# Performance work log

Hardware: AMD Instinct MI355X
Metric: run time of the kernel (lower is better)

The kernel has to match this reference:

```python
import jax, jax.numpy as jnp
import numpy as np

DIM = 1024
NUM_HEADS = 16
HEAD_DIM = DIM // NUM_HEADS
MLP_DIM = 4 * DIM
EPS = 1e-5


def layer_norm(x, g, b):
    mu = jnp.mean(x, axis=-1, keepdims=True)
    var = jnp.mean(jnp.square(x - mu), axis=-1, keepdims=True)
    return (x - mu) * jax.lax.rsqrt(var + EPS) * g + b


def setup_inputs() -> dict:
    key = jax.random.key(0)
    ks = jax.random.split(key, 12)
    B, L = 2, 2048
    s = lambda n: 1.0 / np.sqrt(n)
    return {
        "x": jax.random.normal(ks[0], (B, L, DIM), jnp.float32),
        "attn_mask": jnp.tril(jnp.ones((L, L), jnp.int32))[None, None],  # [1,1,L,L]
        "w_qkv": jax.random.normal(ks[1], (DIM, 3 * DIM), jnp.float32) * s(DIM),
        "b_qkv": jnp.zeros((3 * DIM,), jnp.float32),
        "w_proj": jax.random.normal(ks[2], (DIM, DIM), jnp.float32) * s(DIM),
        "b_proj": jnp.zeros((DIM,), jnp.float32),
        "w_fc1": jax.random.normal(ks[3], (DIM, MLP_DIM), jnp.float32) * s(DIM),
        "b_fc1": jnp.zeros((MLP_DIM,), jnp.float32),
        "w_fc2": jax.random.normal(ks[4], (MLP_DIM, DIM), jnp.float32) * s(MLP_DIM),
        "b_fc2": jnp.zeros((DIM,), jnp.float32),
        "g1": jnp.ones((DIM,), jnp.float32),
        "beta1": jnp.zeros((DIM,), jnp.float32),
        "g2": jnp.ones((DIM,), jnp.float32),
        "beta2": jnp.zeros((DIM,), jnp.float32),
    }


def reference(x, attn_mask, w_qkv, b_qkv, w_proj, b_proj, w_fc1, b_fc1,
              w_fc2, b_fc2, g1, beta1, g2, beta2):
    B, L, D = x.shape
    scale = HEAD_DIM ** -0.5

    # --- attention branch (pre-norm) ---
    h = layer_norm(x, g1, beta1)
    qkv = h @ w_qkv + b_qkv                                  # [B,L,3D]
    qkv = qkv.reshape(B, L, 3, NUM_HEADS, HEAD_DIM)
    q = qkv[:, :, 0].transpose(0, 2, 1, 3)                   # [B,H,L,hd]
    k = qkv[:, :, 1].transpose(0, 2, 1, 3)
    v = qkv[:, :, 2].transpose(0, 2, 1, 3)
    attn = jnp.einsum('bhqd,bhkd->bhqk', q, k) * scale       # [B,H,L,L]
    attn = jnp.where(attn_mask == 0, -jnp.inf, attn)
    attn = jax.nn.softmax(attn, axis=-1)
    y = jnp.einsum('bhqk,bhkd->bhqd', attn, v)               # [B,H,L,hd]
    y = y.transpose(0, 2, 1, 3).reshape(B, L, D)
    y = y @ w_proj + b_proj
    x = x + y

    # --- MLP branch (pre-norm) ---
    h = layer_norm(x, g2, beta2)
    h = jax.nn.gelu(h @ w_fc1 + b_fc1, approximate=False)
    h = h @ w_fc2 + b_fc2
    return x + h
```

## Files before the change

kernel.cpp:

```cpp
#include <hip/hip_runtime.h>
#include <hip/hip_bf16.h>
#include <stdint.h>

typedef unsigned short u16;
typedef __attribute__((ext_vector_type(8))) short bf16x8;
typedef __attribute__((ext_vector_type(4))) short bf16x4;
typedef __attribute__((ext_vector_type(4))) float f32x4;
typedef __attribute__((ext_vector_type(16))) float f32x16;
typedef __attribute__((ext_vector_type(4))) unsigned short u16x4;

#define DEVI static __device__ __forceinline__

DEVI u16 f2bf(float f) {
    unsigned int u = __builtin_bit_cast(unsigned int, f);
    return (u16)((u + 0x7fffu + ((u >> 16) & 1u)) >> 16);
}

DEVI float gelu_f(float v) {
    const float z = 1.5957691216f * (v + 0.044715f * v * v * v);
    return v / (1.0f + __expf(-z));
}

DEVI void async_copy16(const void* g, void* l) {
    __builtin_amdgcn_global_load_lds((const __attribute__((address_space(1))) void*)g,
                                     (__attribute__((address_space(3))) void*)l,
                                     16, 0, 0);
}

__global__ __launch_bounds__(256) void tcvt_kernel(const float* __restrict__ src,
                                                   u16* __restrict__ dst,
                                                   int K, int N) {
    __shared__ float tile[32][33];
    const int k0 = blockIdx.x * 32, n0 = blockIdx.y * 32;
    const int t = threadIdx.x;
    const int c = t & 31, r0 = t >> 5;
#pragma unroll
    for (int p = 0; p < 4; ++p) {
        const int r = r0 + p * 8;
        tile[r][c] = src[(size_t)(k0 + r) * N + n0 + c];
    }
    __syncthreads();
#pragma unroll
    for (int p = 0; p < 4; ++p) {
        const int r = r0 + p * 8;
        dst[(size_t)(n0 + r) * K + k0 + c] = f2bf(tile[c][r]);
    }
}

__global__ __launch_bounds__(256) void ln_kernel(const float* __restrict__ x,
                                                 const float* __restrict__ gw,
                                                 const float* __restrict__ bw,
                                                 u16* __restrict__ out) {
    const int row = blockIdx.x;
    const int t = threadIdx.x;
    const float4 v = ((const float4*)(x + (size_t)row * 1024))[t];
    float s  = v.x + v.y + v.z + v.w;
    float ss = v.x * v.x + v.y * v.y + v.z * v.z + v.w * v.w;
#pragma unroll
    for (int off = 32; off > 0; off >>= 1) {
        s  += __shfl_down(s, off);
        ss += __shfl_down(ss, off);
    }
    __shared__ float red[8];
    const int wv = t >> 6;
    if ((t & 63) == 0) { red[wv] = s; red[4 + wv] = ss; }
    __syncthreads();
    if (t == 0) {
        red[0] = red[0] + red[1] + red[2] + red[3];
        red[4] = red[4] + red[5] + red[6] + red[7];
    }
    __syncthreads();
    const float mean = red[0] * (1.0f / 1024.0f);
    const float var  = red[4] * (1.0f / 1024.0f) - mean * mean;
    const float rstd = rsqrtf(var + 1e-5f);
    const float4 gv = ((const float4*)gw)[t];
    const float4 bv = ((const float4*)bw)[t];
    u16x4 o;
    o[0] = f2bf((v.x - mean) * rstd * gv.x + bv.x);
    o[1] = f2bf((v.y - mean) * rstd * gv.y + bv.y);
    o[2] = f2bf((v.z - mean) * rstd * gv.z + bv.z);
    o[3] = f2bf((v.w - mean) * rstd * gv.w + bv.w);
    ((u16x4*)out)[(size_t)row * 256 + t] = o;
}

DEVI void stage64(const char* g, size_t ldb, char* lds0, int lane, int wv) {
    const int colsw = ((lane & 3) << 4) ^ (lane & 32);
    const int rl = lane >> 2;
#pragma unroll
    for (int i = 0; i < 4; ++i) {
        const int s = wv * 4 + i;
        const int kh = s >> 3, c = s & 7;
        async_copy16(g + (size_t)(c * 16 + rl) * ldb + kh * 64 + colsw,
                     lds0 + s * 1024);
    }
}

template <int EPI, int SPLITK>
__global__ __launch_bounds__(256, 4) void gemmv6(const u16* __restrict__ A,
                                                 const u16* __restrict__ Bt,
                                                 const float* __restrict__ bias,
                                                 void* __restrict__ out0,
                                                 void* __restrict__ out1,
                                                 void* __restrict__ out2,
                                                 int M, int N, int K) {
    __shared__ __align__(16) char As[16384];
    __shared__ __align__(16) char Bs[16384];
    const int tid = threadIdx.x;
    const int lane = tid & 63, wv = tid >> 6;
    const int wr = wv >> 1, wc = wv & 1;
    const int g = lane >> 4, qq = lane & 15;
    const int rdoff = qq * 64 + ((g * 16) ^ ((qq & 8) << 2));

    const int nwg = gridDim.x;
    int id = blockIdx.x;
    id = (id & 7) * (nwg >> 3) + (id >> 3);
    const int MT = M >> 7, NTn = N >> 7;
    const int slice = id / (MT * NTn);
    const int r2 = id % (MT * NTn);
    const int m0 = (r2 % MT) << 7;
    const int n0 = (r2 / MT) << 7;
    const int Ks = K / SPLITK;
    const int NT = Ks >> 6;
    const size_t ldb = (size_t)K * 2;

    const char* pa = (const char*)A + (size_t)m0 * ldb + (size_t)slice * Ks * 2;
    const char* pb = (const char*)Bt + (size_t)n0 * ldb + (size_t)slice * Ks * 2;

    f32x4 acc[4][4] = {};

    for (int t = 0; t < NT; ++t) {
        stage64(pa + (size_t)t * 128, ldb, As, lane, wv);
        stage64(pb + (size_t)t * 128, ldb, Bs, lane, wv);
        __syncthreads();
#pragma unroll
        for (int kh = 0; kh < 2; ++kh) {
            bf16x8 fa[4], fb[4];
#pragma unroll
            for (int fn = 0; fn < 4; ++fn)
                fb[fn] = *(const bf16x8*)(Bs + (kh * 8 + wc * 4 + fn) * 1024 + rdoff);
#pragma unroll
            for (int fm = 0; fm < 4; ++fm)
                fa[fm] = *(const bf16x8*)(As + (kh * 8 + wr * 4 + fm) * 1024 + rdoff);
#pragma unroll
            for (int fm = 0; fm < 4; ++fm)
#pragma unroll
                for (int fn = 0; fn < 4; ++fn)
                    acc[fm][fn] = __builtin_amdgcn_mfma_f32_16x16x32_bf16(fa[fm], fb[fn],
                                                                          acc[fm][fn], 0, 0, 0);
        }
        __syncthreads();
    }

#pragma unroll
    for (int fm = 0; fm < 4; ++fm) {
#pragma unroll
        for (int fn = 0; fn < 4; ++fn) {
            const int mrow = m0 + wr * 64 + fm * 16 + g * 4;
            const int ncol = n0 + wc * 64 + fn * 16 + qq;
            if constexpr (EPI == 0) {
                const float bs = bias[ncol];
                const int sec = ncol >> 10;
                const int hd_ = ncol & 1023;
                const int hh = hd_ >> 6, dd = hd_ & 63;
                if (sec == 2) {
                    const int b_ = mrow >> 11, l_ = mrow & 2047;
                    u16x4 pk;
#pragma unroll
                    for (int r = 0; r < 4; ++r) pk[r] = f2bf(acc[fm][fn][r] + bs);
                    *(u16x4*)((u16*)out2 + ((size_t)((b_ * 16 + hh) * 64 + dd)) * 2048 + l_) = pk;
                } else {
                    u16* dst = (sec == 0) ? (u16*)out0 : (u16*)out1;
                    const float sc = (sec == 0) ? 0.1803368801f : 1.0f;
#pragma unroll
                    for (int r = 0; r < 4; ++r) {
                        const int mr = mrow + r;
                        const int b_ = mr >> 11, l_ = mr & 2047;
                        dst[((size_t)((b_ * 16 + hh) * 2048 + l_)) * 64 + dd] =
                            f2bf((acc[fm][fn][r] + bs) * sc);
                    }
                }
            } else if constexpr (EPI == 2) {
                const float bs = bias[ncol];
                u16* dst = (u16*)out0;
#pragma unroll
                for (int r = 0; r < 4; ++r)
                    dst[(size_t)(mrow + r) * N + ncol] = f2bf(gelu_f(acc[fm][fn][r] + bs));
            } else {
                float* dst = (float*)out0 + (size_t)slice * M * N;
#pragma unroll
                for (int r = 0; r < 4; ++r)
                    dst[(size_t)(mrow + r) * N + ncol] = acc[fm][fn][r];
            }
        }
    }
}

template <int SPLIT>
__global__ __launch_bounds__(256) void reduceN_kernel(const float* __restrict__ p,
                                                      const float* __restrict__ bias,
                                                      const float* __restrict__ res,
                                                      float* __restrict__ out,
                                                      int MN4, int N4) {
    const int i = blockIdx.x * 256 + threadIdx.x;
    float4 s = ((const float4*)p)[i];
#pragma unroll
    for (int s2 = 1; s2 < SPLIT; ++s2) {
        const float4 q = ((const float4*)p)[(size_t)s2 * MN4 + i];
        s.x += q.x; s.y += q.y; s.z += q.z; s.w += q.w;
    }
    const float4 r = ((const float4*)res)[i];
    const float4 bs = ((const float4*)bias)[i & (N4 - 1)];
    float4 o;
    o.x = s.x + r.x + bs.x;
    o.y = s.y + r.y + bs.y;
    o.z = s.z + r.z + bs.z;
    o.w = s.w + r.w + bs.w;
    ((float4*)out)[i] = o;
}

DEVI void stage_kv(const char* kbase, const char* vbase, int key0,
                   u16* ksm, u16* vsm, int wv, int lane) {
#pragma unroll
    for (int i = 0; i < 2; ++i) {
        const int c = wv + i * 4;
        const int off = c * 1024 + lane * 16;
        const int row = off >> 7;
        const int scol = (off & 127) ^ ((row & 7) << 4);
        async_copy16(kbase + (size_t)key0 * 128 + (size_t)row * 128 + scol,
                     (char*)ksm + c * 1024);
    }
#pragma unroll
    for (int i = 0; i < 2; ++i) {
        const int c = wv + i * 4;
        const int row = c * 8 + (lane >> 3);
        const int scol = ((lane & 7) * 16) ^ ((row & 7) << 4);
        async_copy16(vbase + (size_t)row * 4096 + (size_t)key0 * 2 + scol,
                     (char*)vsm + c * 1024);
    }
}

__global__ __launch_bounds__(256, 4) void attn32_seg(const u16* __restrict__ Q,
                                                     const u16* __restrict__ Kk,
                                                     const u16* __restrict__ Vt,
                                                     float* __restrict__ opart,
                                                     float2* __restrict__ ml) {
    const int bh = blockIdx.z;
    const int seg = blockIdx.y;
    const int qb = gridDim.x - 1 - blockIdx.x;
    const int tid = threadIdx.x;
    const int wv = tid >> 6, lane = tid & 63;
    const int hi = lane >> 5, qc = lane & 31;

    __shared__ __align__(16) u16 Ksm[4096];
    __shared__ __align__(16) u16 Vsm[4096];
    __shared__ __align__(16) u16 Pl[4][32 * 68];

    const char* Kb = (const char*)(Kk + (size_t)bh * 2048 * 64);
    const char* Vb = (const char*)(Vt + (size_t)bh * 64 * 2048);
    u16* Pw = &Pl[wv][0];

    const int q0w = qb * 128 + wv * 32;
    const int qg = q0w + qc;
    const int nt_half = qb + 1;
    const int kt_begin = seg ? nt_half : 0;
    const int kt_end = seg ? (2 * qb + 2) : nt_half;
    const int ntw = min(kt_end, 2 * qb + (wv >> 1) + 1);

    bf16x8 qf[4];
    {
        const u16* Qp = Q + ((size_t)bh * 2048 + qg) * 64;
#pragma unroll
        for (int c = 0; c < 4; ++c)
            qf[c] = *(const bf16x8*)(Qp + c * 16 + hi * 8);
    }

    f32x16 oacc[2];
#pragma unroll
    for (int r = 0; r < 16; ++r) { oacc[0][r] = 0.0f; oacc[1][r] = 0.0f; }
    float m_run = -60000.0f, l_run = 0.0f;

    for (int kt = kt_begin; kt < kt_end; ++kt) {
        const int key0 = kt * 64;
        stage_kv(Kb, Vb, key0, Ksm, Vsm, wv, lane);
        __syncthreads();
        if (kt < ntw) {
            f32x16 sacc[2];
#pragma unroll
            for (int r = 0; r < 16; ++r) { sacc[0][r] = 0.0f; sacc[1][r] = 0.0f; }
#pragma unroll
            for (int c = 0; c < 4; ++c) {
#pragma unroll
                for (int kb = 0; kb < 2; ++kb) {
                    const int kr = kb * 32 + qc;
                    const bf16x8 ak = *(const bf16x8*)((const char*)Ksm + kr * 128 +
                                          ((c * 32 + hi * 16) ^ ((kr & 7) << 4)));
                    sacc[kb] = __builtin_amdgcn_mfma_f32_32x32x16_bf16(ak, qf[c],
                                                                       sacc[kb], 0, 0, 0);
                }
            }
            float pmax = -1e30f;
            if (key0 + 63 > q0w) {
#pragma unroll
                for (int kb = 0; kb < 2; ++kb)
#pragma unroll
                    for (int r = 0; r < 16; ++r) {
                        const int key = key0 + kb * 32 + (r & 3) + 8 * (r >> 2) + 4 * hi;
                        float s = sacc[kb][r];
                        if (key > qg) s = -1e30f;
                        sacc[kb][r] = s;
                        pmax = fmaxf(pmax, s);
                    }
            } else {
#pragma unroll
                for (int kb = 0; kb < 2; ++kb)
#pragma unroll
                    for (int r = 0; r < 16; ++r) pmax = fmaxf(pmax, sacc[kb][r]);
            }
            pmax = fmaxf(pmax, __shfl_xor(pmax, 32));
            if (pmax > m_run + 11.0f) {
                const float alpha = __builtin_amdgcn_exp2f(m_run - pmax);
#pragma unroll
                for (int r = 0; r < 16; ++r) { oacc[0][r] *= alpha; oacc[1][r] *= alpha; }
                l_run *= alpha;
                m_run = pmax;
            }
            float lsum = 0.0f;
#pragma unroll
            for (int kb = 0; kb < 2; ++kb)
#pragma unroll
                for (int j = 0; j < 4; ++j) {
                    u16x4 pk4;
#pragma unroll
                    for (int t = 0; t < 4; ++t) {
                        const float e = __builtin_amdgcn_exp2f(sacc[kb][j * 4 + t] - m_run);
                        lsum += e;
                        pk4[t] = f2bf(e);
                    }
                    *(u16x4*)(Pw + qc * 68 + kb * 32 + j * 8 + 4 * hi) = pk4;
                }
            lsum += __shfl_xor(lsum, 32);
            l_run += lsum;
#pragma unroll
            for (int c = 0; c < 4; ++c) {
                const u16* pp = Pw + qc * 68 + c * 16 + hi * 8;
                union { bf16x8 v; struct { bf16x4 lo; bf16x4 hi2; } s; } u;
                u.s.lo  = *(const bf16x4*)(pp);
                u.s.hi2 = *(const bf16x4*)(pp + 4);
                const bf16x8 pf = u.v;
#pragma unroll
                for (int db = 0; db < 2; ++db) {
                    const int dr = db * 32 + qc;
                    const bf16x8 av = *(const bf16x8*)((const char*)Vsm + dr * 128 +
                                          ((c * 32 + hi * 16) ^ ((dr & 7) << 4)));
                    oacc[db] = __builtin_amdgcn_mfma_f32_32x32x16_bf16(av, pf,
                                                                       oacc[db], 0, 0, 0);
                }
            }
        }
        __syncthreads();
    }

    const size_t row = (size_t)seg * 65536 + (size_t)bh * 2048 + qg;
    float* op = opart + row * 64;
#pragma unroll
    for (int db = 0; db < 2; ++db)
#pragma unroll
        for (int j = 0; j < 4; ++j) {
            float4 v;
            v.x = oacc[db][j * 4 + 0];
            v.y = oacc[db][j * 4 + 1];
            v.z = oacc[db][j * 4 + 2];
            v.w = oacc[db][j * 4 + 3];
            *(float4*)(op + db * 32 + j * 8 + 4 * hi) = v;
        }
    if (hi == 0) { float2 t; t.x = m_run; t.y = l_run; ml[row] = t; }
}

__global__ __launch_bounds__(256) void attn_comb(const float* __restrict__ opart,
                                                 const float2* __restrict__ ml,
                                                 u16* __restrict__ Y) {
    const int idx = blockIdx.x * 256 + threadIdx.x;
    const int row = idx >> 4, d4 = idx & 15;
    const float2 ml0 = ml[row];
    const float2 ml1 = ml[65536 + row];
    const float m = fmaxf(ml0.x, ml1.x);
    const float w0 = __builtin_amdgcn_exp2f(ml0.x - m);
    const float w1 = __builtin_amdgcn_exp2f(ml1.x - m);
    const float inv = 1.0f / (ml0.y * w0 + ml1.y * w1);
    const float4 a = ((const float4*)opart)[(size_t)row * 16 + d4];
    const float4 b = ((const float4*)opart)[(size_t)(65536 + row) * 16 + d4];
    const int bh = row >> 11, q = row & 2047;
    const int b_ = bh >> 4, hh = bh & 15;
    u16x4 o;
    o[0] = f2bf((a.x * w0 + b.x * w1) * inv);
    o[1] = f2bf((a.y * w0 + b.y * w1) * inv);
    o[2] = f2bf((a.z * w0 + b.z * w1) * inv);
    o[3] = f2bf((a.w * w0 + b.w * w1) * inv);
    *(u16x4*)(Y + ((size_t)(b_ * 2048 + q)) * 1024 + hh * 64 + d4 * 4) = o;
}

extern "C" void kernel_launch(void* const* d_in, const int* in_sizes, int n_in,
                              void* d_out, int out_size, void* d_ws, size_t ws_size,
                              hipStream_t stream) {
    (void)in_sizes; (void)n_in; (void)out_size;
    const float* x      = (const float*)d_in[0];
    const float* w_qkv  = (const float*)d_in[2];
    const float* b_qkv  = (const float*)d_in[3];
    const float* w_proj = (const float*)d_in[4];
    const float* b_proj = (const float*)d_in[5];
    const float* w_fc1  = (const float*)d_in[6];
    const float* b_fc1  = (const float*)d_in[7];
    const float* w_fc2  = (const float*)d_in[8];
    const float* b_fc2  = (const float*)d_in[9];
    const float* g1     = (const float*)d_in[10];
    const float* be1    = (const float*)d_in[11];
    const float* g2     = (const float*)d_in[12];
    const float* be2    = (const float*)d_in[13];

    char* ws = (char*)d_ws;
    size_t off = 0;
    auto alloc = [&](size_t bytes) { size_t r = off; off += (bytes + 255) & ~(size_t)255; return r; };
    u16*   wt_qkv = (u16*)(ws + alloc((size_t)3072 * 1024 * 2));
    u16*   wt_prj = (u16*)(ws + alloc((size_t)1024 * 1024 * 2));
    u16*   wt_fc1 = (u16*)(ws + alloc((size_t)4096 * 1024 * 2));
    u16*   wt_fc2 = (u16*)(ws + alloc((size_t)1024 * 4096 * 2));
    u16*   hbuf   = (u16*)(ws + alloc((size_t)4096 * 1024 * 2));
    float* x1     = (float*)(ws + alloc((size_t)4096 * 1024 * 4));
    char*  big    = ws + alloc((size_t)33554432);
    u16* qb  = (u16*)(big);
    u16* kb  = (u16*)(big + 8388608);
    u16* vtb = (u16*)(big + 16777216);
    u16* yb  = (u16*)(big + 25165824);
    u16* act = (u16*)(big);
    if (off > ws_size) return;
    const size_t part_need = (size_t)4 * 4096 * 1024 * 4 + (size_t)2 * 65536 * 8;
    if ((ws_size - off) < part_need) return;
    float*  part  = (float*)(ws + off);
    float*  opart = part;
    float2* mlp   = (float2*)(ws + off + (size_t)4 * 4096 * 1024 * 4);

    const dim3 blk(256);
    tcvt_kernel<<<dim3(32, 96), blk, 0, stream>>>(w_qkv, wt_qkv, 1024, 3072);
    tcvt_kernel<<<dim3(32, 32), blk, 0, stream>>>(w_proj, wt_prj, 1024, 1024);
    tcvt_kernel<<<dim3(32, 128), blk, 0, stream>>>(w_fc1, wt_fc1, 1024, 4096);
    tcvt_kernel<<<dim3(128, 32), blk, 0, stream>>>(w_fc2, wt_fc2, 4096, 1024);

    ln_kernel<<<dim3(4096), blk, 0, stream>>>(x, g1, be1, hbuf);
    gemmv6<0, 1><<<dim3(768), blk, 0, stream>>>(hbuf, wt_qkv, b_qkv,
                                                qb, kb, vtb, 4096, 3072, 1024);
    attn32_seg<<<dim3(16, 2, 32), blk, 0, stream>>>(qb, kb, vtb, opart, mlp);
    attn_comb<<<dim3(4096), blk, 0, stream>>>(opart, mlp, yb);
    gemmv6<4, 2><<<dim3(512), blk, 0, stream>>>(yb, wt_prj, nullptr,
                                                part, nullptr, nullptr, 4096, 1024, 1024);
    reduceN_kernel<2><<<dim3(4096), blk, 0, stream>>>(part, b_proj, x, x1, 1048576, 256);
    ln_kernel<<<dim3(4096), blk, 0, stream>>>(x1, g2, be2, hbuf);
    gemmv6<2, 1><<<dim3(1024), blk, 0, stream>>>(hbuf, wt_fc1, b_fc1,
                                                 act, nullptr, nullptr, 4096, 4096, 1024);
    gemmv6<4, 4><<<dim3(1024), blk, 0, stream>>>(act, wt_fc2, nullptr,
                                                 part, nullptr, nullptr, 4096, 1024, 4096);
    reduceN_kernel<4><<<dim3(4096), blk, 0, stream>>>(part, b_fc2, x1, (float*)d_out,
                                                      1048576, 256);
}
```

Measured before the change: 254.7 us.

## Split causal attention into four key segments and add 256x128 GEMM for FC1

Result: slower. 261.0 us (+2.5%).

```diff
diff --git a/kernel.cpp b/kernel.cpp
--- a/kernel.cpp
+++ b/kernel.cpp
@@ -195,6 +195,96 @@
     }
 }
 
+template <int EPI, int SPLITK>
+__global__ __launch_bounds__(512, 4) void gemm256(const u16* __restrict__ A,
+                                                  const u16* __restrict__ Bt,
+                                                  const float* __restrict__ bias,
+                                                  void* __restrict__ out0,
+                                                  int M, int N, int K) {
+    __shared__ __align__(16) char As[32768];
+    __shared__ __align__(16) char Bs[16384];
+    const int tid = threadIdx.x;
+    const int lane = tid & 63, wv = tid >> 6;
+    const int wr = wv >> 1, wc = wv & 1;
+    const int g = lane >> 4, qq = lane & 15;
+    const int rdoff = qq * 64 + ((g * 16) ^ ((qq & 8) << 2));
+    const int colsw = ((lane & 3) << 4) ^ (lane & 32);
+    const int rl = lane >> 2;
+
+    const int nwg = gridDim.x;
+    int id = blockIdx.x;
+    id = (id & 7) * (nwg >> 3) + (id >> 3);
+    const int MT = M >> 8, NTn = N >> 7;
+    const int slice = id / (MT * NTn);
+    const int r2 = id % (MT * NTn);
+    const int m0 = (r2 % MT) << 8;
+    const int n0 = (r2 / MT) << 7;
+    const int Ks = K / SPLITK;
+    const int NT = Ks >> 6;
+    const size_t ldb = (size_t)K * 2;
+
+    const char* pa = (const char*)A + (size_t)m0 * ldb + (size_t)slice * Ks * 2;
+    const char* pb = (const char*)Bt + (size_t)n0 * ldb + (size_t)slice * Ks * 2;
+
+    f32x4 acc[4][4] = {};
+
+    for (int t = 0; t < NT; ++t) {
+        const char* ga = pa + (size_t)t * 128;
+        const char* gb = pb + (size_t)t * 128;
+#pragma unroll
+        for (int i = 0; i < 4; ++i) {
+            const int s = wv * 4 + i;
+            const int kh = s >> 4, c = s & 15;
+            async_copy16(ga + (size_t)(c * 16 + rl) * ldb + kh * 64 + colsw, As + s * 1024);
+        }
+#pragma unroll
+        for (int i = 0; i < 2; ++i) {
+            const int s = wv * 2 + i;
+            const int kh = s >> 3, c = s & 7;
+            async_copy16(gb + (size_t)(c * 16 + rl) * ldb + kh * 64 + colsw, Bs + s * 1024);
+        }
+        __syncthreads();
+#pragma unroll
+        for (int kh = 0; kh < 2; ++kh) {
+            bf16x8 fa[4], fb[4];
+#pragma unroll
+            for (int fn = 0; fn < 4; ++fn)
+                fb[fn] = *(const bf16x8*)(Bs + (kh * 8 + wc * 4 + fn) * 1024 + rdoff);
+#pragma unroll
+            for (int fm = 0; fm < 4; ++fm)
+                fa[fm] = *(const bf16x8*)(As + (kh * 16 + wr * 4 + fm) * 1024 + rdoff);
+#pragma unroll
+            for (int fm = 0; fm < 4; ++fm)
+#pragma unroll
+                for (int fn = 0; fn < 4; ++fn)
+                    acc[fm][fn] = __builtin_amdgcn_mfma_f32_16x16x32_bf16(fa[fm], fb[fn],
+                                                                          acc[fm][fn], 0, 0, 0);
+        }
+        __syncthreads();
+    }
+
+#pragma unroll
+    for (int fm = 0; fm < 4; ++fm) {
+#pragma unroll
+        for (int fn = 0; fn < 4; ++fn) {
+            const int mrow = m0 + wr * 64 + fm * 16 + g * 4;
+            const int ncol = n0 + wc * 64 + fn * 16 + qq;
+            if constexpr (EPI == 2) {
+                const float bs = bias[ncol];
+                u16* dst = (u16*)out0;
+#pragma unroll
+                for (int r = 0; r < 4; ++r)
+                    dst[(size_t)(mrow + r) * N + ncol] = f2bf(gelu_f(acc[fm][fn][r] + bs));
+            } else {
+                float* dst = (float*)out0 + (size_t)slice * M * N;
+#pragma unroll
+                for (int r = 0; r < 4; ++r)
+                    dst[(size_t)(mrow + r) * N + ncol] = acc[fm][fn][r];
+            }
+        }
+    }
+}
+
 template <int SPLIT>
 __global__ __launch_bounds__(256) void reduceN_kernel(const float* __restrict__ p,
                                                       const float* __restrict__ bias,
@@ -261,9 +351,9 @@
 
     const int q0w = qb * 128 + wv * 32;
     const int qg = q0w + qc;
-    const int nt_half = qb + 1;
-    const int kt_begin = seg ? nt_half : 0;
-    const int kt_end = seg ? (2 * qb + 2) : nt_half;
+    const int T = 2 * qb + 2;
+    const int kt_begin = (seg * T) >> 2;
+    const int kt_end = ((seg + 1) * T) >> 2;
     const int ntw = min(kt_end, 2 * qb + (wv >> 1) + 1);
 
     bf16x8 qf[4];
@@ -376,26 +466,32 @@
     if (hi == 0) { float2 t; t.x = m_run; t.y = l_run; ml[row] = t; }
 }
 
-__global__ __launch_bounds__(256) void attn_comb(const float* __restrict__ opart,
-                                                 const float2* __restrict__ ml,
-                                                 u16* __restrict__ Y) {
+__global__ __launch_bounds__(256) void attn_comb4(const float* __restrict__ opart,
+                                                  const float2* __restrict__ ml,
+                                                  u16* __restrict__ Y) {
     const int idx = blockIdx.x * 256 + threadIdx.x;
     const int row = idx >> 4, d4 = idx & 15;
-    const float2 ml0 = ml[row];
-    const float2 ml1 = ml[65536 + row];
-    const float m = fmaxf(ml0.x, ml1.x);
-    const float w0 = __builtin_amdgcn_exp2f(ml0.x - m);
-    const float w1 = __builtin_amdgcn_exp2f(ml1.x - m);
-    const float inv = 1.0f / (ml0.y * w0 + ml1.y * w1);
-    const float4 a = ((const float4*)opart)[(size_t)row * 16 + d4];
-    const float4 b = ((const float4*)opart)[(size_t)(65536 + row) * 16 + d4];
+    float2 m_l[4];
+#pragma unroll
+    for (int s = 0; s < 4; ++s) m_l[s] = ml[(size_t)s * 65536 + row];
+    float m = fmaxf(fmaxf(m_l[0].x, m_l[1].x), fmaxf(m_l[2].x, m_l[3].x));
+    float w[4], lsum = 0.0f;
+#pragma unroll
+    for (int s = 0; s < 4; ++s) { w[s] = __builtin_amdgcn_exp2f(m_l[s].x - m); lsum += m_l[s].y * w[s]; }
+    const float inv = 1.0f / lsum;
+    float4 acc = {0.0f, 0.0f, 0.0f, 0.0f};
+#pragma unroll
+    for (int s = 0; s < 4; ++s) {
+        const float4 a = ((const float4*)opart)[((size_t)s * 65536 + row) * 16 + d4];
+        acc.x += a.x * w[s]; acc.y += a.y * w[s]; acc.z += a.z * w[s]; acc.w += a.w * w[s];
+    }
     const int bh = row >> 11, q = row & 2047;
     const int b_ = bh >> 4, hh = bh & 15;
     u16x4 o;
-    o[0] = f2bf((a.x * w0 + b.x * w1) * inv);
-    o[1] = f2bf((a.y * w0 + b.y * w1) * inv);
-    o[2] = f2bf((a.z * w0 + b.z * w1) * inv);
-    o[3] = f2bf((a.w * w0 + b.w * w1) * inv);
+    o[0] = f2bf(acc.x * inv);
+    o[1] = f2bf(acc.y * inv);
+    o[2] = f2bf(acc.z * inv);
+    o[3] = f2bf(acc.w * inv);
     *(u16x4*)(Y + ((size_t)(b_ * 2048 + q)) * 1024 + hh * 64 + d4 * 4) = o;
 }
 
@@ -433,7 +529,7 @@
     u16* yb  = (u16*)(big + 25165824);
     u16* act = (u16*)(big);
     if (off > ws_size) return;
-    const size_t part_need = (size_t)4 * 4096 * 1024 * 4 + (size_t)2 * 65536 * 8;
+    const size_t part_need = (size_t)4 * 4096 * 1024 * 4 + (size_t)4 * 65536 * 8;
     if ((ws_size - off) < part_need) return;
     float*  part  = (float*)(ws + off);
     float*  opart = part;
@@ -448,14 +544,14 @@
     ln_kernel<<<dim3(4096), blk, 0, stream>>>(x, g1, be1, hbuf);
     gemmv6<0, 1><<<dim3(768), blk, 0, stream>>>(hbuf, wt_qkv, b_qkv,
                                                 qb, kb, vtb, 4096, 3072, 1024);
-    attn32_seg<<<dim3(16, 2, 32), blk, 0, stream>>>(qb, kb, vtb, opart, mlp);
-    attn_comb<<<dim3(4096), blk, 0, stream>>>(opart, mlp, yb);
+    attn32_seg<<<dim3(16, 4, 32), blk, 0, stream>>>(qb, kb, vtb, opart, mlp);
+    attn_comb4<<<dim3(4096), blk, 0, stream>>>(opart, mlp, yb);
     gemmv6<4, 2><<<dim3(512), blk, 0, stream>>>(yb, wt_prj, nullptr,
                                                 part, nullptr, nullptr, 4096, 1024, 1024);
     reduceN_kernel<2><<<dim3(4096), blk, 0, stream>>>(part, b_proj, x, x1, 1048576, 256);
     ln_kernel<<<dim3(4096), blk, 0, stream>>>(x1, g2, be2, hbuf);
-    gemmv6<2, 1><<<dim3(1024), blk, 0, stream>>>(hbuf, wt_fc1, b_fc1,
-                                                 act, nullptr, nullptr, 4096, 4096, 1024);
+    gemm256<2, 1><<<dim3(512), dim3(512), 0, stream>>>(hbuf, wt_fc1, b_fc1,
+                                                       act, 4096, 4096, 1024);
     gemmv6<4, 4><<<dim3(1024), blk, 0, stream>>>(act, wt_fc2, nullptr,
                                                  part, nullptr, nullptr, 4096, 1024, 4096);
     reduceN_kernel<4><<<dim3(4096), blk, 0, stream>>>(part, b_fc2, x1, (float*)d_out,
```
